# Kernel optimization log

Hardware: AMD Instinct MI355X
Metric: run time of the kernel (lower is better)

The kernel has to match this reference:

```python
import jax, jax.numpy as jnp
import numpy as np

K_FEATURES = 512
V_FEATURES = 512
MEMORY_SIZE = 131072
N_QUERIES = 2048
ITEMS_PER_QUERY = 32


def setup_inputs() -> dict:
    key = jax.random.key(0)
    kq, kk, kv = jax.random.split(key, 3)
    q = jax.random.normal(kq, (N_QUERIES, K_FEATURES), dtype=jnp.float32)
    k_memory = jax.random.normal(kk, (MEMORY_SIZE, K_FEATURES), dtype=jnp.float32)
    v_memory = jax.random.normal(kv, (MEMORY_SIZE, V_FEATURES), dtype=jnp.float32)
    return {"q": q, "k_memory": k_memory, "v_memory": v_memory, "items_per_query": ITEMS_PER_QUERY}


def reference(q, k_memory, v_memory, items_per_query):
    # faiss.IndexFlatIP: exact inner-product search -> top-k by q @ K^T
    scores = jnp.einsum('nd,md->nm', q, k_memory)  # [n, memory_size]
    _, indices = jax.lax.top_k(scores, items_per_query)  # [n, i]
    flat_idx = indices.reshape(-1)  # '(n i)' as in the torch rearrange
    k = k_memory[flat_idx]  # [n*i, k_features]
    v = v_memory[flat_idx]  # [n*i, v_features]
    return (k, v)
```

## Files before the change

### kernel.cpp

```cpp
#include <hip/hip_runtime.h>
#include <float.h>

#define NQ     2048
#define DIM    512
#define MSZ    131072
#define TOPK   32
#define QT     128
#define BN     128
#define BK     64
#define NITER  (DIM / BK)
#define STRIP  128
#define NSTRIP (MSZ / STRIP)
#define TOPS   6
#define CPQ    (NSTRIP * TOPS)
#define NV     (CPQ / 64)
#define MERGE  128
#define SCW    65

typedef float  f32x4  __attribute__((ext_vector_type(4)));

__device__ __forceinline__ unsigned umx(unsigned a, unsigned b) { return a > b ? a : b; }
__device__ __forceinline__ unsigned umn(unsigned a, unsigned b) { return a < b ? a : b; }

__device__ __forceinline__ unsigned f32_to_e4m3(float f) {
    union { float f; unsigned u; } v; v.f = f;
    const unsigned s = (v.u >> 24) & 0x80u;
    unsigned mag = v.u & 0x7FFFFFFFu;
    if (mag < 0x3C800000u) return s;
    if (mag > 0x43D00000u) return s | 0x7Eu;
    const unsigned r = mag + 0x7FFFFu + ((mag >> 20) & 1u);
    return s | (((r >> 23) - 120u) << 3) | ((r >> 20) & 7u);
}

__device__ __forceinline__ void gload16(const void* g, void* l) {
    __builtin_amdgcn_global_load_lds(
        (const __attribute__((address_space(1))) unsigned int*)g,
        (__attribute__((address_space(3))) unsigned int*)l, 16, 0, 0);
}

#define INS6(pk)                                                             \
    {                                                                        \
        const unsigned t0 = umx(s0, pk), t1 = umx(s1, pk), t2 = umx(s2, pk), \
                       t3 = umx(s3, pk), t4 = umx(s4, pk), t5 = umx(s5, pk); \
        s0 = umn(s1, t0); s1 = umn(s2, t1); s2 = umn(s3, t2);                \
        s3 = umn(s4, t3); s4 = umn(s5, t4); s5 = t5;                         \
    }

__global__ __launch_bounds__(256) void k0_convert_fp8(
    const float* __restrict__ src, unsigned* __restrict__ dst, int n4)
{
    int i = blockIdx.x * blockDim.x + threadIdx.x;
    const int stride = gridDim.x * blockDim.x;
    const float4* s4 = reinterpret_cast<const float4*>(src);
    for (; i < n4; i += stride) {
        const float4 v = s4[i];
        dst[i] = f32_to_e4m3(v.x) | (f32_to_e4m3(v.y) << 8) |
                 (f32_to_e4m3(v.z) << 16) | (f32_to_e4m3(v.w) << 24);
    }
}

__global__ __launch_bounds__(256, 3) void k1_score_select(
    const unsigned char* __restrict__ qf8, const unsigned char* __restrict__ kf8,
    unsigned* __restrict__ cand)
{
    const int s   = blockIdx.x;
    const int xcd = s & 7;
    const int idx = s >> 3;
    const int qt  = idx & 15;
    const int bn  = xcd * (NSTRIP / 8) + (idx >> 4);

    const int tid  = threadIdx.x;
    const int w    = tid >> 6;
    const int lane = tid & 63;
    const int l15  = lane & 15;
    const int kgrp = lane >> 4;
    const int wq   = w >> 1;
    const int wr   = w & 1;
    const int srow = lane >> 2;
    const int sslt = lane & 3;

    __shared__ __align__(16) char lds[49152];

    f32x4 acc[4][4];
    #pragma unroll
    for (int mt = 0; mt < 4; ++mt)
        #pragma unroll
        for (int nt = 0; nt < 4; ++nt)
            acc[mt][nt] = (f32x4){0.f, 0.f, 0.f, 0.f};

    const int rA0 = w * 32 + srow;
    const int rA1 = rA0 + 16;
    const int sl0 = (sslt ^ ((rA0 >> 1) & 3)) << 4;
    const int sl1 = (sslt ^ ((rA1 >> 1) & 3)) << 4;
    const unsigned char* sA0 = qf8 + ((size_t)(qt * QT + rA0) << 9) + sl0;
    const unsigned char* sA1 = qf8 + ((size_t)(qt * QT + rA1) << 9) + sl1;
    const unsigned char* sB0 = kf8 + ((size_t)(bn * BN + rA0) << 9) + sl0;
    const unsigned char* sB1 = kf8 + ((size_t)(bn * BN + rA1) << 9) + sl1;
    char* const dA = lds + w * 2048;
    char* const dB = lds + 24576 + w * 2048;

    int offA[4][2], offB[4][2];
    #pragma unroll
    for (int mt = 0; mt < 4; ++mt) {
        const int ra = wq * 64 + mt * 16 + l15;
        const int ka = (ra >> 1) & 3;
        const int rb = wr * 64 + mt * 16 + l15;
        const int kb = (rb >> 1) & 3;
        const int sub = (kgrp & 1) * 8;
        #pragma unroll
        for (int ks = 0; ks < 2; ++ks) {
            const int slot = (ks << 1) | (kgrp >> 1);
            offA[mt][ks] = ra * 64 + ((slot ^ ka) << 4) + sub;
            offB[mt][ks] = rb * 64 + ((slot ^ kb) << 4) + sub;
        }
    }

#define STAGE(bsel)                                                          \
    {                                                                        \
        gload16(sA0, dA + (bsel) * 8192);                                    \
        gload16(sA1, dA + (bsel) * 8192 + 1024);                             \
        gload16(sB0, dB + (bsel) * 8192);                                    \
        gload16(sB1, dB + (bsel) * 8192 + 1024);                             \
        sA0 += 64; sA1 += 64; sB0 += 64; sB1 += 64;                          \
    }

    STAGE(0);
    STAGE(1);
    asm volatile("s_waitcnt vmcnt(4)" ::: "memory");
    __builtin_amdgcn_s_barrier();

    #pragma unroll
    for (int kk = 0; kk < NITER; ++kk) {
        const int buf = kk % 3;
        if (kk < NITER - 2) STAGE((kk + 2) % 3);

        const char* bA = lds + buf * 8192;
        const char* bB = lds + 24576 + buf * 8192;
        #pragma unroll
        for (int ks = 0; ks < 2; ++ks) {
            long a[4], b[4];
            #pragma unroll
            for (int mt = 0; mt < 4; ++mt)
                a[mt] = *reinterpret_cast<const long*>(bA + offA[mt][ks]);
            #pragma unroll
            for (int nt = 0; nt < 4; ++nt)
                b[nt] = *reinterpret_cast<const long*>(bB + offB[nt][ks]);

            __builtin_amdgcn_s_setprio(1);
            #pragma unroll
            for (int mt = 0; mt < 4; ++mt)
                #pragma unroll
                for (int nt = 0; nt < 4; ++nt)
                    acc[mt][nt] = __builtin_amdgcn_mfma_f32_16x16x32_fp8_fp8(
                        a[mt], b[nt], acc[mt][nt], 0, 0, 0);
            __builtin_amdgcn_s_setprio(0);
        }

        if (kk < NITER - 2) {
            asm volatile("s_waitcnt vmcnt(4)" ::: "memory");
        } else {
            asm volatile("s_waitcnt vmcnt(0)" ::: "memory");
        }
        __builtin_amdgcn_s_barrier();
    }
#undef STAGE

    unsigned* sc32 = reinterpret_cast<unsigned*>(lds);
    #pragma unroll
    for (int mt = 0; mt < 4; ++mt)
        #pragma unroll
        for (int nt = 0; nt < 4; ++nt) {
            const int q0 = wq * 64 + mt * 16 + kgrp * 4;
            const int rl = wr * 64 + nt * 16 + l15;
            #pragma unroll
            for (int rp = 0; rp < 2; ++rp) {
                unsigned pk;
                asm("v_cvt_pk_bf16_f32 %0, %1, %2"
                    : "=v"(pk)
                    : "v"(acc[mt][nt][2 * rp]), "v"(acc[mt][nt][2 * rp + 1]));
                const unsigned sgn = pk & 0x80008000u;
                const unsigned m   = sgn >> 15;
                const unsigned msk = (m << 16) - m;
                const unsigned ord = pk ^ (msk | 0x80008000u);
                ((unsigned short*)(sc32 + (q0 + 2 * rp) * SCW))[rl] =
                    (unsigned short)ord;
                ((unsigned short*)(sc32 + (q0 + 2 * rp + 1) * SCW))[rl] =
                    (unsigned short)(ord >> 16);
            }
        }
    __syncthreads();

    const int q = tid & 127;
    const int h = tid >> 7;
    unsigned s0 = 0, s1 = 0, s2 = 0, s3 = 0, s4 = 0, s5 = 0;
    {
        const unsigned* rowp = sc32 + (size_t)q * SCW + h * 32;
        #pragma unroll
        for (int u = 0; u < 32; ++u) {
            const unsigned p = rowp[u];
            const unsigned pos0 = 127u - 2u * (unsigned)(h * 32 + u);
            const unsigned pk0 = (p << 16) | pos0;
            const unsigned pk1 = (p & 0xFFFF0000u) | (pos0 - 1u);
            INS6(pk0);
            INS6(pk1);
        }
    }
    __syncthreads();

    unsigned* selb = reinterpret_cast<unsigned*>(lds);
    if (h) {
        unsigned* o = selb + q * 7;
        o[0] = s0; o[1] = s1; o[2] = s2; o[3] = s3; o[4] = s4; o[5] = s5;
    }
    __syncthreads();
    if (h) return;

    {
        const unsigned* other = selb + q * 7;
        #pragma unroll
        for (int u = 0; u < 6; ++u) {
            const unsigned pk = other[u];
            INS6(pk);
        }
        const int qid = qt * QT + q;
        unsigned* base = cand + (size_t)qid * CPQ + (size_t)bn * TOPS;
        base[0] = s5; base[1] = s4; base[2] = s3;
        base[3] = s2; base[4] = s1; base[5] = s0;
    }
}

__global__ __launch_bounds__(256) void k2_merge_rescore(
    const float* __restrict__ q, const float* __restrict__ kmem,
    const unsigned* __restrict__ cand, int* __restrict__ final_idx)
{
    const int w    = threadIdx.x >> 6;
    const int lane = threadIdx.x & 63;
    const int qid  = blockIdx.x * 4 + w;

    __shared__ int   rows_s[4][MERGE];
    __shared__ float scs_s[4][MERGE];

    unsigned v[NV];
    const uint4* cp4 = reinterpret_cast<const uint4*>(cand + (size_t)qid * CPQ);
    #pragma unroll
    for (int j = 0; j < NV / 4; ++j) {
        const uint4 t = cp4[j * 64 + lane];
        v[j * 4 + 0] = t.x; v[j * 4 + 1] = t.y;
        v[j * 4 + 2] = t.z; v[j * 4 + 3] = t.w;
    }
    const int kBits[17] = {25,24,23,22,21,20,19,18,17,16,6,5,4,3,2,1,0};
    unsigned P = 0xC0000000u;
    #pragma unroll
    for (int bi = 0; bi < 17; ++bi) {
        const unsigned trial = P | (1u << kBits[bi]);
        int cnt = 0;
        #pragma unroll
        for (int j = 0; j < NV; ++j) cnt += (v[j] >= trial);
        #pragma unroll
        for (int m = 1; m < 64; m <<= 1) cnt += __shfl_xor(cnt, m);
        if (cnt >= MERGE) P = trial;
    }
    int gt = 0, eq = 0;
    #pragma unroll
    for (int j = 0; j < NV; ++j) { gt += (v[j] > P); eq += (v[j] == P); }
    int pgt = gt, peq = eq;
    #pragma unroll
    for (int m = 1; m < 64; m <<= 1) {
        const int ag = __shfl_up(pgt, m);
        const int ae = __shfl_up(peq, m);
        if (lane >= m) { pgt += ag; peq += ae; }
    }
    const int totGT = __shfl(pgt, 63);
    pgt -= gt; peq -= eq;
    const int quotaEq = MERGE - totGT;
    {
        int sgt = pgt, seq = peq;
        #pragma unroll
        for (int j = 0; j < NV; ++j) {
            const int off   = (j & ~3) * 64 + lane * 4 + (j & 3);
            const int strip = off / TOPS;
            const int row   = strip * STRIP + (STRIP - 1) - (int)(v[j] & 127u);
            if (v[j] > P) {
                rows_s[w][sgt++] = row;
            } else if (v[j] == P) {
                if (seq < quotaEq) rows_s[w][totGT + seq] = row;
                seq++;
            }
        }
    }
    __syncthreads();

    {
#pragma clang fp contract(off)
        const float4* qr = reinterpret_cast<const float4*>(q + (size_t)qid * DIM);
        const int ra = rows_s[w][lane];
        const int rb = rows_s[w][lane + 64];
        const float4* ka = reinterpret_cast<const float4*>(kmem + (size_t)ra * DIM);
        const float4* kb = reinterpret_cast<const float4*>(kmem + (size_t)rb * DIM);
        float sa = 0.f, sb = 0.f;
        for (int d4 = 0; d4 < DIM / 4; ++d4) {
            const float4 qv = qr[d4];
            const float4 av = ka[d4];
            const float4 bv = kb[d4];
            sa = __builtin_fmaf(qv.x, av.x, sa); sb = __builtin_fmaf(qv.x, bv.x, sb);
            sa = __builtin_fmaf(qv.y, av.y, sa); sb = __builtin_fmaf(qv.y, bv.y, sb);
            sa = __builtin_fmaf(qv.z, av.z, sa); sb = __builtin_fmaf(qv.z, bv.z, sb);
            sa = __builtin_fmaf(qv.w, av.w, sa); sb = __builtin_fmaf(qv.w, bv.w, sb);
        }
        scs_s[w][lane]      = sa;
        scs_s[w][lane + 64] = sb;
    }
    __syncthreads();

    float m0 = scs_s[w][lane],      m1 = scs_s[w][lane + 64];
    const int rr0 = rows_s[w][lane], rr1 = rows_s[w][lane + 64];
    for (int sel = 0; sel < TOPK; ++sel) {
        float bs; int bi;
        if (m0 > m1 || (m0 == m1 && rr0 < rr1)) { bs = m0; bi = rr0; }
        else                                    { bs = m1; bi = rr1; }
        #pragma unroll
        for (int m = 1; m < 64; m <<= 1) {
            const float os = __shfl_xor(bs, m);
            const int   oi = __shfl_xor(bi, m);
            if (os > bs || (os == bs && oi < bi)) { bs = os; bi = oi; }
        }
        if (lane == 0) final_idx[qid * TOPK + sel] = bi;
        if (rr0 == bi) m0 = -FLT_MAX;
        if (rr1 == bi) m1 = -FLT_MAX;
    }
}

__global__ __launch_bounds__(128) void k3_gather(
    const float* __restrict__ kmem, const float* __restrict__ vmem,
    const int* __restrict__ final_idx, float* __restrict__ out)
{
    const int b = blockIdx.x;
    const int t = threadIdx.x;
    const int idx = final_idx[b];
    const float4* kr = reinterpret_cast<const float4*>(kmem + (size_t)idx * DIM);
    const float4* vr = reinterpret_cast<const float4*>(vmem + (size_t)idx * DIM);
    float4* ok = reinterpret_cast<float4*>(out + (size_t)b * DIM);
    float4* ov = reinterpret_cast<float4*>(out + (size_t)NQ * TOPK * DIM + (size_t)b * DIM);
    ok[t] = kr[t];
    ov[t] = vr[t];
}

extern "C" void kernel_launch(void* const* d_in, const int* in_sizes, int n_in,
                              void* d_out, int out_size, void* d_ws, size_t ws_size,
                              hipStream_t stream)
{
    const float* q    = (const float*)d_in[0];
    const float* kmem = (const float*)d_in[1];
    const float* vmem = (const float*)d_in[2];
    float* out = (float*)d_out;

    unsigned char* base = (unsigned char*)d_out;
    unsigned char* kf8 = base;
    unsigned char* qf8 = base + (size_t)MSZ * DIM;
    unsigned* cand = (unsigned*)(base + (size_t)MSZ * DIM + (size_t)NQ * DIM);
    int* final_idx = (int*)d_ws;

    k0_convert_fp8<<<4096, 256, 0, stream>>>(kmem, (unsigned*)kf8, MSZ * DIM / 4);
    k0_convert_fp8<<<256, 256, 0, stream>>>(q, (unsigned*)qf8, NQ * DIM / 4);
    k1_score_select<<<(NQ / QT) * NSTRIP, 256, 0, stream>>>(qf8, kf8, cand);
    k2_merge_rescore<<<NQ / 4, 256, 0, stream>>>(q, kmem, cand, final_idx);
    k3_gather<<<NQ * TOPK, 128, 0, stream>>>(kmem, vmem, final_idx, out);
}
```

Before: 548.8 us.

## Switch scoring GEMM to 32x32x64 scaled FP8 MFMA and shorten radix select

Replaces the 16x16x32 FP8 MFMA tiles with 32x32x64 scaled f8f6f4 MFMA instructions, using unit scales. This reduces the number of MFMA issues and LDS fragment loads per K-step, and the score write-out is remapped to the 32x32 accumulator layout. The merge kernel's radix threshold search now stops at the bf16 score bits and no longer refines the low position bits, treating ties within the same score as the equal bucket. That saves seven reduction rounds but changes the order in which tied candidates are admitted.

```diff
diff --git a/kernel.cpp b/kernel.cpp
--- a/kernel.cpp
+++ b/kernel.cpp
@@ -17,7 +17,10 @@
 #define MERGE  128
 #define SCW    65
 
-typedef float  f32x4  __attribute__((ext_vector_type(4)));
+typedef float    f32x4  __attribute__((ext_vector_type(4)));
+typedef float    f32x16 __attribute__((ext_vector_type(16)));
+typedef int      v8i    __attribute__((ext_vector_type(8)));
+typedef unsigned u32x4v __attribute__((ext_vector_type(4)));
 
 __device__ __forceinline__ unsigned umx(unsigned a, unsigned b) { return a > b ? a : b; }
 __device__ __forceinline__ unsigned umn(unsigned a, unsigned b) { return a < b ? a : b; }
@@ -72,8 +75,8 @@
     const int tid  = threadIdx.x;
     const int w    = tid >> 6;
     const int lane = tid & 63;
-    const int l15  = lane & 15;
-    const int kgrp = lane >> 4;
+    const int l31  = lane & 31;
+    const int h64  = lane >> 5;
     const int wq   = w >> 1;
     const int wr   = w & 1;
     const int srow = lane >> 2;
@@ -81,12 +84,12 @@
 
     __shared__ __align__(16) char lds[49152];
 
-    f32x4 acc[4][4];
-    #pragma unroll
-    for (int mt = 0; mt < 4; ++mt)
-        #pragma unroll
-        for (int nt = 0; nt < 4; ++nt)
-            acc[mt][nt] = (f32x4){0.f, 0.f, 0.f, 0.f};
+    f32x16 acc[2][2];
+    #pragma unroll
+    for (int mt = 0; mt < 2; ++mt)
+        #pragma unroll
+        for (int nt = 0; nt < 2; ++nt)
+            acc[mt][nt] = (f32x16)(0.f);
 
     const int rA0 = w * 32 + srow;
     const int rA1 = rA0 + 16;
@@ -99,19 +102,17 @@
     char* const dA = lds + w * 2048;
     char* const dB = lds + 24576 + w * 2048;
 
-    int offA[4][2], offB[4][2];
-    #pragma unroll
-    for (int mt = 0; mt < 4; ++mt) {
-        const int ra = wq * 64 + mt * 16 + l15;
+    int offA[2][2], offB[2][2];
+    #pragma unroll
+    for (int mt = 0; mt < 2; ++mt) {
+        const int ra = wq * 64 + mt * 32 + l31;
         const int ka = (ra >> 1) & 3;
-        const int rb = wr * 64 + mt * 16 + l15;
+        const int rb = wr * 64 + mt * 32 + l31;
         const int kb = (rb >> 1) & 3;
-        const int sub = (kgrp & 1) * 8;
-        #pragma unroll
-        for (int ks = 0; ks < 2; ++ks) {
-            const int slot = (ks << 1) | (kgrp >> 1);
-            offA[mt][ks] = ra * 64 + ((slot ^ ka) << 4) + sub;
-            offB[mt][ks] = rb * 64 + ((slot ^ kb) << 4) + sub;
+        #pragma unroll
+        for (int p = 0; p < 2; ++p) {
+            offA[mt][p] = ra * 64 + (((2 * h64 + p) ^ ka) << 4);
+            offB[mt][p] = rb * 64 + (((2 * h64 + p) ^ kb) << 4);
         }
     }
 
@@ -136,25 +137,33 @@
 
         const char* bA = lds + buf * 8192;
         const char* bB = lds + 24576 + buf * 8192;
-        #pragma unroll
-        for (int ks = 0; ks < 2; ++ks) {
-            long a[4], b[4];
+        v8i a[2], b[2];
+        #pragma unroll
+        for (int mt = 0; mt < 2; ++mt) {
+            union { u32x4v h[2]; v8i v; } u;
+            u.h[0] = *reinterpret_cast<const u32x4v*>(bA + offA[mt][0]);
+            u.h[1] = *reinterpret_cast<const u32x4v*>(bA + offA[mt][1]);
+            a[mt] = u.v;
+        }
+        #pragma unroll
+        for (int nt = 0; nt < 2; ++nt) {
+            union { u32x4v h[2]; v8i v; } u;
+            u.h[0] = *reinterpret_cast<const u32x4v*>(bB + offB[nt][0]);
+            u.h[1] = *reinterpret_cast<const u32x4v*>(bB + offB[nt][1]);
+            b[nt] = u.v;
+        }
+
+        __builtin_amdgcn_s_setprio(1);
+        #pragma unroll
+        for (int mt = 0; mt < 2; ++mt)
             #pragma unroll
-            for (int mt = 0; mt < 4; ++mt)
-                a[mt] = *reinterpret_cast<const long*>(bA + offA[mt][ks]);
-            #pragma unroll
-            for (int nt = 0; nt < 4; ++nt)
-                b[nt] = *reinterpret_cast<const long*>(bB + offB[nt][ks]);
-
-            __builtin_amdgcn_s_setprio(1);
-            #pragma unroll
-            for (int mt = 0; mt < 4; ++mt)
-                #pragma unroll
-                for (int nt = 0; nt < 4; ++nt)
-                    acc[mt][nt] = __builtin_amdgcn_mfma_f32_16x16x32_fp8_fp8(
-                        a[mt], b[nt], acc[mt][nt], 0, 0, 0);
-            __builtin_amdgcn_s_setprio(0);
-        }
+            for (int nt = 0; nt < 2; ++nt)
+                acc[mt][nt] = __builtin_amdgcn_mfma_scale_f32_32x32x64_f8f6f4(
+                    a[mt], b[nt], acc[mt][nt],
+                    0, 0,
+                    0, 0x7F7F7F7F,
+                    0, 0x7F7F7F7F);
+        __builtin_amdgcn_s_setprio(0);
 
         if (kk < NITER - 2) {
             asm volatile("s_waitcnt vmcnt(4)" ::: "memory");
@@ -167,24 +176,24 @@
 
     unsigned* sc32 = reinterpret_cast<unsigned*>(lds);
     #pragma unroll
-    for (int mt = 0; mt < 4; ++mt)
-        #pragma unroll
-        for (int nt = 0; nt < 4; ++nt) {
-            const int q0 = wq * 64 + mt * 16 + kgrp * 4;
-            const int rl = wr * 64 + nt * 16 + l15;
+    for (int mt = 0; mt < 2; ++mt)
+        #pragma unroll
+        for (int nt = 0; nt < 2; ++nt) {
+            const int rl = wr * 64 + nt * 32 + l31;
             #pragma unroll
-            for (int rp = 0; rp < 2; ++rp) {
+            for (int i = 0; i < 8; ++i) {
+                const int qv = wq * 64 + mt * 32 + ((2 * i) & 3) + 8 * (i >> 1)
+                               + 4 * h64;
                 unsigned pk;
                 asm("v_cvt_pk_bf16_f32 %0, %1, %2"
                     : "=v"(pk)
-                    : "v"(acc[mt][nt][2 * rp]), "v"(acc[mt][nt][2 * rp + 1]));
+                    : "v"(acc[mt][nt][2 * i]), "v"(acc[mt][nt][2 * i + 1]));
                 const unsigned sgn = pk & 0x80008000u;
                 const unsigned m   = sgn >> 15;
                 const unsigned msk = (m << 16) - m;
                 const unsigned ord = pk ^ (msk | 0x80008000u);
-                ((unsigned short*)(sc32 + (q0 + 2 * rp) * SCW))[rl] =
-                    (unsigned short)ord;
-                ((unsigned short*)(sc32 + (q0 + 2 * rp + 1) * SCW))[rl] =
+                ((unsigned short*)(sc32 + qv * SCW))[rl] = (unsigned short)ord;
+                ((unsigned short*)(sc32 + (qv + 1) * SCW))[rl] =
                     (unsigned short)(ord >> 16);
             }
         }
@@ -248,11 +257,10 @@
         v[j * 4 + 0] = t.x; v[j * 4 + 1] = t.y;
         v[j * 4 + 2] = t.z; v[j * 4 + 3] = t.w;
     }
-    const int kBits[17] = {25,24,23,22,21,20,19,18,17,16,6,5,4,3,2,1,0};
     unsigned P = 0xC0000000u;
     #pragma unroll
-    for (int bi = 0; bi < 17; ++bi) {
-        const unsigned trial = P | (1u << kBits[bi]);
+    for (int b = 25; b >= 16; --b) {
+        const unsigned trial = P | (1u << b);
         int cnt = 0;
         #pragma unroll
         for (int j = 0; j < NV; ++j) cnt += (v[j] >= trial);
@@ -260,9 +268,13 @@
         for (int m = 1; m < 64; m <<= 1) cnt += __shfl_xor(cnt, m);
         if (cnt >= MERGE) P = trial;
     }
+    const unsigned Pp = P + 0x10000u;
     int gt = 0, eq = 0;
     #pragma unroll
-    for (int j = 0; j < NV; ++j) { gt += (v[j] > P); eq += (v[j] == P); }
+    for (int j = 0; j < NV; ++j) {
+        gt += (v[j] >= Pp);
+        eq += (v[j] >= P) && (v[j] < Pp);
+    }
     int pgt = gt, peq = eq;
     #pragma unroll
     for (int m = 1; m < 64; m <<= 1) {
@@ -280,9 +292,9 @@
             const int off   = (j & ~3) * 64 + lane * 4 + (j & 3);
             const int strip = off / TOPS;
             const int row   = strip * STRIP + (STRIP - 1) - (int)(v[j] & 127u);
-            if (v[j] > P) {
+            if (v[j] >= Pp) {
                 rows_s[w][sgt++] = row;
-            } else if (v[j] == P) {
+            } else if (v[j] >= P) {
                 if (seq < quotaEq) rows_s[w][totGT + seq] = row;
                 seq++;
             }
```

Result: faster. 515.0 us (median of 2 runs) (-6.1%).
